# Kernel tuning notes

Measured on AMD Instinct MI355X. Metric: run time of the kernel, lower is better.

## Reference

```python
import jax, jax.numpy as jnp
import numpy as np

B, N, C, H = 4, 2048, 1024, 16
D = C // H  # head_dim = 64
SCALE = D ** -0.5


def setup_inputs() -> dict:
    key = jax.random.key(0)
    ks = jax.random.split(key, 7)
    # freqs_cis = exp(i*theta): unit-modulus rotations, as in standard RoPE
    theta = jax.random.uniform(ks[1], (B, N, D // 2), jnp.float32, 0.0, 2 * np.pi)
    return {
        "x": jax.random.normal(ks[0], (B, N, C), jnp.float32),
        "freqs_cos": jnp.cos(theta),
        "freqs_sin": jnp.sin(theta),
        "attn_mask": jax.random.normal(ks[2], (1, 1, N, N), jnp.float32) * 0.1,
        "Wqkv": jax.random.normal(ks[3], (3 * C, C), jnp.float32) * (C ** -0.5),
        "Wproj": jax.random.normal(ks[4], (C, C), jnp.float32) * (C ** -0.5),
        "bproj": jnp.zeros((C,), jnp.float32),
    }


def _rope(t, cos, sin):
    # t: [B,H,N,D]; cos/sin: [B,1,N,D/2]; complex multiply on interleaved pairs
    tr = t.reshape(*t.shape[:-1], D // 2, 2)
    t0, t1 = tr[..., 0], tr[..., 1]
    out = jnp.stack([t0 * cos - t1 * sin, t0 * sin + t1 * cos], axis=-1)
    return out.reshape(t.shape)


def reference(x, freqs_cos, freqs_sin, attn_mask, Wqkv, Wproj, bproj):
    qkv = x @ Wqkv.T  # [B,N,3C]
    qkv = qkv.reshape(B, N, 3, H, D).transpose(2, 0, 3, 1, 4)  # [3,B,H,N,D]
    q, k, v = qkv[0], qkv[1], qkv[2]
    cos = freqs_cos[:, None]  # [B,1,N,D/2]
    sin = freqs_sin[:, None]
    q = _rope(q, cos, sin)
    k = _rope(k, cos, sin)
    attn = jnp.einsum("bhnd,bhmd->bhnm", q * SCALE, k) + attn_mask
    attn = jax.nn.softmax(attn, axis=-1)
    out = jnp.einsum("bhnm,bhmd->bhnd", attn, v)  # [B,H,N,D]
    out = out.transpose(0, 2, 1, 3).reshape(B, N, C)
    return out @ Wproj.T + bproj
```

## Files before the change

### kernel.cpp

```cpp
#include <hip/hip_runtime.h>
#include <hip/hip_bf16.h>
#include <stdint.h>


typedef __bf16 bf16;
typedef __bf16 bf16x4 __attribute__((ext_vector_type(4)));
typedef __bf16 bf16x8 __attribute__((ext_vector_type(8)));
typedef float  f32x4  __attribute__((ext_vector_type(4)));
typedef float  f32x16 __attribute__((ext_vector_type(16)));
typedef int    int4v  __attribute__((ext_vector_type(4)));

#define MFMA16(a, b, c) __builtin_amdgcn_mfma_f32_16x16x32_bf16((a), (b), (c), 0, 0, 0)
#define MFMA32(a, b, c) __builtin_amdgcn_mfma_f32_32x32x16_bf16((a), (b), (c), 0, 0, 0)

__device__ __forceinline__ bf16x4 cvt4s(float a, float b, float c, float d) {
  bf16x4 r;
  r[0] = (bf16)a; r[1] = (bf16)b; r[2] = (bf16)c; r[3] = (bf16)d;
  return r;
}
__device__ __forceinline__ bf16x8 cvt8(f32x4 a, f32x4 b) {
  bf16x8 r;
  r[0] = (bf16)a[0]; r[1] = (bf16)a[1]; r[2] = (bf16)a[2]; r[3] = (bf16)a[3];
  r[4] = (bf16)b[0]; r[5] = (bf16)b[1]; r[6] = (bf16)b[2]; r[7] = (bf16)b[3];
  return r;
}
__device__ __forceinline__ void gload16(const void* g, void* l) {
  __builtin_amdgcn_global_load_lds((const __attribute__((address_space(1))) void*)g,
                                   (__attribute__((address_space(3))) void*)l, 16, 0, 0);
}

__global__ __launch_bounds__(256)
void cvt_all(const float* __restrict__ x,  bf16* __restrict__ xb,
             const float* __restrict__ wq, bf16* __restrict__ wqb,
             const float* __restrict__ wp, bf16* __restrict__ wpb,
             const float* __restrict__ mk, bf16* __restrict__ mkb)
{
  const int bi = blockIdx.x;
  const float* src; bf16* dst; float scale = 1.0f; size_t off;
  if (bi < 4096)      { src = x;  dst = xb;  off = (size_t)bi * 2048; }
  else if (bi < 5632) { src = wq; dst = wqb; off = (size_t)(bi - 4096) * 2048; }
  else if (bi < 6144) { src = wp; dst = wpb; off = (size_t)(bi - 5632) * 2048; }
  else { src = mk; dst = mkb; off = (size_t)(bi - 6144) * 2048;
         scale = 1.4426950408889634f; }
  const size_t i = off + (size_t)threadIdx.x * 8;
  f32x4 a = *(const f32x4*)(src + i) * scale;
  f32x4 b = *(const f32x4*)(src + i + 4) * scale;
  *(bf16x8*)(dst + i) = cvt8(a, b);
}

template<int MODE>
__global__ __launch_bounds__(256)
void gemm_bt(const bf16* __restrict__ A, const bf16* __restrict__ B,
             void* __restrict__ O0, bf16* __restrict__ O1, bf16* __restrict__ O2,
             const float* __restrict__ bias)
{
  constexpr int K = 1024;
  __shared__ __attribute__((aligned(16))) bf16 S[MODE == 0 ? 17408 : 16384];
  bf16* As = S;
  bf16* Bs = S + 128 * 64;
  const int tid = threadIdx.x, lane = tid & 63, wid = tid >> 6;
  const int m0 = blockIdx.x * 128, n0 = blockIdx.y * 128;
  const int wm = (wid >> 1) * 64, wn = (wid & 1) * 64;
  const int l15 = lane & 15, lg = lane >> 4;

  f32x4 acc[4][4] = {};

  for (int k0 = 0; k0 < K; k0 += 64) {
#pragma unroll
    for (int c = 0; c < 4; ++c) {
      const int seg = wid * 4 + c;
      const int o = seg * 1024 + lane * 16;
      const int row = o >> 7, colb = o & 127;
      gload16((const char*)B + (((size_t)(n0 + row) * K + k0) << 1) + colb,
              (char*)Bs + seg * 1024);
      gload16((const char*)A + (((size_t)(m0 + row) * K + k0) << 1) + colb,
              (char*)As + seg * 1024);
    }
    __syncthreads();

    bf16x8 af[4][2], bb[4][2];
#pragma unroll
    for (int i = 0; i < 4; ++i)
#pragma unroll
      for (int kk = 0; kk < 2; ++kk) {
        af[i][kk] = *(const bf16x8*)(As + (wm + i * 16 + l15) * 64 + kk * 32 + lg * 8);
        bb[i][kk] = *(const bf16x8*)(Bs + (wn + i * 16 + l15) * 64 + kk * 32 + lg * 8);
      }
#pragma unroll
    for (int mi = 0; mi < 4; ++mi)
#pragma unroll
      for (int ni = 0; ni < 4; ++ni)
#pragma unroll
        for (int kk = 0; kk < 2; ++kk)
          acc[mi][ni] = MFMA16(af[mi][kk], bb[ni][kk], acc[mi][ni]);
    __syncthreads();
  }

  if (MODE == 0) {
    bf16* T = S;
#pragma unroll
    for (int mi = 0; mi < 4; ++mi)
#pragma unroll
      for (int ni = 0; ni < 4; ++ni)
#pragma unroll
        for (int r = 0; r < 4; ++r)
          T[(wm + mi * 16 + lg * 4 + r) * 136 + wn + ni * 16 + l15] =
              (bf16)acc[mi][ni][r];
    __syncthreads();

    const int s = n0 >> 10;
    const int h0 = (n0 >> 6) & 15;
    if (s < 2) {
      bf16* dst = (s == 0) ? (bf16*)O0 : O1;
      const int nl = tid >> 1, ch = (tid & 1) * 64;
      const int row = m0 + nl, b = row >> 11, n = row & 2047;
#pragma unroll
      for (int j = 0; j < 8; ++j) {
        const int c = ch + j * 8;
        const int h = h0 + (c >> 6), d0 = c & 63;
        const int ds = (s == 1) ? (d0 ^ ((n & 7) << 3)) : d0;
        *(int4v*)(dst + (((size_t)(b * 16 + h) * 2048) + n) * 64 + ds) =
            *(const int4v*)(T + nl * 136 + c);
      }
    } else {
      const int c = tid >> 1, nh = (tid & 1) * 64;
      const int h = h0 + (c >> 6), d = c & 63;
      const int b = m0 >> 11, nb = m0 & 2047;
#pragma unroll
      for (int j = 0; j < 8; ++j) {
        const int n8 = nh + j * 8;
        __attribute__((aligned(16))) bf16 tmp[8];
#pragma unroll
        for (int i = 0; i < 8; ++i) tmp[i] = T[(n8 + i) * 136 + c];
        const int ng = nb + n8;
        const int nswz = (ng & ~63) | ((ng & 63) ^ ((d & 7) << 3));
        *(int4v*)(O2 + ((size_t)(b * 16 + h) * 64 + d) * 2048 + nswz) =
            *(const int4v*)tmp;
      }
    }
  } else {
#pragma unroll
    for (int mi = 0; mi < 4; ++mi)
#pragma unroll
      for (int ni = 0; ni < 4; ++ni)
#pragma unroll
        for (int r = 0; r < 4; ++r) {
          const int row = m0 + wm + mi * 16 + lg * 4 + r;
          const int col = n0 + wn + ni * 16 + l15;
          ((float*)O0)[(size_t)row * 1024 + col] = acc[mi][ni][r] + bias[col];
        }
  }
}

__global__ __launch_bounds__(256)
void rope_k(bf16* __restrict__ Q, bf16* __restrict__ K,
            const float* __restrict__ C, const float* __restrict__ S)
{
  constexpr float SL = 0.125f * 1.4426950408889634f;
  const int gid = blockIdx.x * 256 + threadIdx.x;
  const int part = gid & 3;
  const int rowid = gid >> 2;
  const int n = rowid & 2047;
  const int b = rowid >> 15;
  const size_t cb0 = ((size_t)(b * 2048 + n)) * 32;

  __attribute__((aligned(16))) bf16 buf[16];

  {
    float cf[8], sf[8];
    *(f32x4*)cf = *(const f32x4*)(C + cb0 + part * 8);
    *(f32x4*)(cf + 4) = *(const f32x4*)(C + cb0 + part * 8 + 4);
    *(f32x4*)sf = *(const f32x4*)(S + cb0 + part * 8);
    *(f32x4*)(sf + 4) = *(const f32x4*)(S + cb0 + part * 8 + 4);

    bf16* qp = Q + (size_t)rowid * 64 + part * 16;
    *(int4v*)buf = *(const int4v*)qp;
    *(int4v*)(buf + 8) = *(const int4v*)(qp + 8);
#pragma unroll
    for (int j = 0; j < 8; ++j) {
      const float t0 = (float)buf[2 * j], t1 = (float)buf[2 * j + 1];
      buf[2 * j]     = (bf16)((t0 * cf[j] - t1 * sf[j]) * SL);
      buf[2 * j + 1] = (bf16)((t0 * sf[j] + t1 * cf[j]) * SL);
    }
    *(int4v*)qp = *(int4v*)buf;
    *(int4v*)(qp + 8) = *(int4v*)(buf + 8);
  }

  {
    const int sg = n & 7;
    bf16* kp = K + (size_t)rowid * 64 + part * 16;
    *(int4v*)buf = *(const int4v*)kp;
    *(int4v*)(buf + 8) = *(const int4v*)(kp + 8);
#pragma unroll
    for (int gi = 0; gi < 2; ++gi) {
      const int lg = (2 * part + gi) ^ sg;
      const f32x4 c4 = *(const f32x4*)(C + cb0 + lg * 4);
      const f32x4 s4 = *(const f32x4*)(S + cb0 + lg * 4);
#pragma unroll
      for (int m = 0; m < 4; ++m) {
        const float t0 = (float)buf[gi * 8 + 2 * m];
        const float t1 = (float)buf[gi * 8 + 2 * m + 1];
        buf[gi * 8 + 2 * m]     = (bf16)(t0 * c4[m] - t1 * s4[m]);
        buf[gi * 8 + 2 * m + 1] = (bf16)(t0 * s4[m] + t1 * c4[m]);
      }
    }
    *(int4v*)kp = *(int4v*)buf;
    *(int4v*)(kp + 8) = *(int4v*)(buf + 8);
  }
}

template<int MM>
__global__ __launch_bounds__(512, 4)
void attn_k(const bf16* __restrict__ Q, const bf16* __restrict__ K,
            const bf16* __restrict__ VT, const void* __restrict__ Mv,
            bf16* __restrict__ O)
{
  constexpr float LOG2E = 1.4426950408889634f;
  constexpr int NT = 32;
  __shared__ __attribute__((aligned(16))) bf16 SH[18432];

  const int tid = threadIdx.x, lane = tid & 63, w = tid >> 6;
  const int bh = blockIdx.x;
  const int q0 = blockIdx.y * 256;
  const int b = bh >> 4, h = bh & 15;
  const int l31 = lane & 31, hi = lane >> 5;
  const int swz = (l31 & 7) << 3;

  const bf16* Qb = Q + (size_t)bh * 2048 * 64;
  const bf16* Kb = K + (size_t)bh * 2048 * 64;
  const bf16* Vb = VT + (size_t)bh * 64 * 2048;
  const float* Mqf = (const float*)Mv + (size_t)(q0 + w * 32 + l31) * 2048;
  const bf16*  Mqb = (const bf16*)Mv  + (size_t)(q0 + w * 32 + l31) * 2048;

  bf16x8 qf[4];
  {
    const bf16* qr = Qb + (size_t)(q0 + w * 32 + l31) * 64 + 8 * hi;
#pragma unroll
    for (int j = 0; j < 4; ++j) qf[j] = *(const bf16x8*)(qr + 16 * j);
  }

  f32x16 o[2] = {{0,0,0,0,0,0,0,0,0,0,0,0,0,0,0,0},
                 {0,0,0,0,0,0,0,0,0,0,0,0,0,0,0,0}};
  float li = 0.f;

#define STAGE_TILE(KVN, BUFSEL) do {                                          \
    bf16* Ktn = SH + (BUFSEL) * 8192;                                         \
    bf16* Vtn = Ktn + 4096;                                                   \
    gload16((const char*)Kb + (((size_t)(KVN) * 64 + tid * 8) << 1),          \
            (char*)Ktn + w * 1024);                                           \
    gload16((const char*)Vb +                                                 \
                (((size_t)(tid >> 3) * 2048 + (KVN) + (tid & 7) * 8) << 1),   \
            (char*)Vtn + w * 1024);                                           \
  } while (0)

  bf16x4 mkb_cur[2][4], mkb_nxt[2][4];

  STAGE_TILE(0, 0);
  if (MM == 1) {
#pragma unroll
    for (int sub = 0; sub < 2; ++sub)
#pragma unroll
      for (int rg = 0; rg < 4; ++rg)
        mkb_cur[sub][rg] = *(const bf16x4*)(Mqb + 32 * sub + 8 * rg + 4 * hi);
  }
  __syncthreads();

  for (int t = 0; t < NT; ++t) {
    bf16* Kt = SH + (t & 1) * 8192;
    bf16* Vt = Kt + 4096;

    if (t + 1 < NT) {
      const int kvn = (t + 1) * 64;
      STAGE_TILE(kvn, (t + 1) & 1);
      if (MM == 1) {
#pragma unroll
        for (int sub = 0; sub < 2; ++sub)
#pragma unroll
          for (int rg = 0; rg < 4; ++rg)
            mkb_nxt[sub][rg] = *(const bf16x4*)(Mqb + kvn + 32 * sub + 8 * rg + 4 * hi);
      }
    }
    f32x4 mkf[2][4];
    if (MM == 0) {
      const int kv0 = t * 64;
#pragma unroll
      for (int sub = 0; sub < 2; ++sub)
#pragma unroll
        for (int rg = 0; rg < 4; ++rg)
          mkf[sub][rg] = *(const f32x4*)(Mqf + kv0 + 32 * sub + 8 * rg + 4 * hi);
    }

#pragma unroll
    for (int sub = 0; sub < 2; ++sub) {
      f32x16 s;
#pragma unroll
      for (int rg = 0; rg < 4; ++rg)
#pragma unroll
        for (int i = 0; i < 4; ++i)
          s[4 * rg + i] = (MM == 0) ? mkf[sub][rg][i] * LOG2E
                                    : (float)mkb_cur[sub][rg][i];
      __builtin_amdgcn_s_setprio(1);
#pragma unroll
      for (int j = 0; j < 4; ++j) {
        const bf16x8 kf = *(const bf16x8*)(
            Kt + (sub * 32 + l31) * 64 + ((16 * j + 8 * hi) ^ swz));
        s = MFMA32(kf, qf[j], s);
      }
      __builtin_amdgcn_s_setprio(0);

      float rs = 0.f;
#pragma unroll
      for (int e = 0; e < 16; ++e) {
        const float p = __builtin_exp2f(s[e]);
        s[e] = p;
        rs += p;
      }
      rs += __shfl_xor(rs, 32);
      li += rs;

      uint32_t pk0, pk1, pk2, pk3, pk4, pk5, pk6, pk7;
      asm("v_cvt_pk_bf16_f32 %0, %1, %2" : "=v"(pk0) : "v"(s[0]),  "v"(s[1]));
      asm("v_cvt_pk_bf16_f32 %0, %1, %2" : "=v"(pk1) : "v"(s[2]),  "v"(s[3]));
      asm("v_cvt_pk_bf16_f32 %0, %1, %2" : "=v"(pk2) : "v"(s[4]),  "v"(s[5]));
      asm("v_cvt_pk_bf16_f32 %0, %1, %2" : "=v"(pk3) : "v"(s[6]),  "v"(s[7]));
      asm("v_cvt_pk_bf16_f32 %0, %1, %2" : "=v"(pk4) : "v"(s[8]),  "v"(s[9]));
      asm("v_cvt_pk_bf16_f32 %0, %1, %2" : "=v"(pk5) : "v"(s[10]), "v"(s[11]));
      asm("v_cvt_pk_bf16_f32 %0, %1, %2" : "=v"(pk6) : "v"(s[12]), "v"(s[13]));
      asm("v_cvt_pk_bf16_f32 %0, %1, %2" : "=v"(pk7) : "v"(s[14]), "v"(s[15]));
      asm("v_permlane32_swap_b32 %0, %1" : "+v"(pk0), "+v"(pk2));
      asm("v_permlane32_swap_b32 %0, %1" : "+v"(pk1), "+v"(pk3));
      asm("v_permlane32_swap_b32 %0, %1" : "+v"(pk4), "+v"(pk6));
      asm("v_permlane32_swap_b32 %0, %1" : "+v"(pk5), "+v"(pk7));
      uint32_t pau[2][4] = {{pk0, pk1, pk2, pk3}, {pk4, pk5, pk6, pk7}};
      bf16x8 pa[2];
      __builtin_memcpy(&pa[0], pau[0], 16);
      __builtin_memcpy(&pa[1], pau[1], 16);

      __builtin_amdgcn_s_setprio(1);
#pragma unroll
      for (int kh = 0; kh < 2; ++kh)
#pragma unroll
        for (int dblk = 0; dblk < 2; ++dblk) {
          const bf16x8 vf = *(const bf16x8*)(
              Vt + (dblk * 32 + l31) * 64 + ((sub * 32 + kh * 16 + 8 * hi) ^ swz));
          o[dblk] = MFMA32(vf, pa[kh], o[dblk]);
        }
      __builtin_amdgcn_s_setprio(0);
    }

    if (MM == 1 && t + 1 < NT) {
#pragma unroll
      for (int sub = 0; sub < 2; ++sub)
#pragma unroll
        for (int rg = 0; rg < 4; ++rg)
          mkb_cur[sub][rg] = mkb_nxt[sub][rg];
    }
    __syncthreads();
  }
#undef STAGE_TILE

  const float inv = 1.f / li;
  bf16* ow = SH + w * 2304;
#pragma unroll
  for (int dblk = 0; dblk < 2; ++dblk)
#pragma unroll
    for (int rg = 0; rg < 4; ++rg)
      *(bf16x4*)(ow + l31 * 72 + dblk * 32 + 8 * rg + 4 * hi) =
          cvt4s(o[dblk][4 * rg] * inv, o[dblk][4 * rg + 1] * inv,
                o[dblk][4 * rg + 2] * inv, o[dblk][4 * rg + 3] * inv);
  asm volatile("s_waitcnt lgkmcnt(0)" ::: "memory");
  __builtin_amdgcn_sched_barrier(0);
#pragma unroll
  for (int p = 0; p < 4; ++p) {
    const int row = p * 8 + (lane >> 3);
    const int n = q0 + w * 32 + row;
    const int4v v = *(const int4v*)(ow + row * 72 + (lane & 7) * 8);
    *(int4v*)(O + ((size_t)b * 2048 + n) * 1024 + h * 64 + (lane & 7) * 8) = v;
  }
}

extern "C" void kernel_launch(void* const* d_in, const int* in_sizes, int n_in,
                              void* d_out, int out_size, void* d_ws, size_t ws_size,
                              hipStream_t stream)
{
  (void)in_sizes; (void)n_in; (void)out_size;
  const float* x     = (const float*)d_in[0];
  const float* fcos  = (const float*)d_in[1];
  const float* fsin  = (const float*)d_in[2];
  const float* mask  = (const float*)d_in[3];
  const float* wqkv  = (const float*)d_in[4];
  const float* wproj = (const float*)d_in[5];
  const float* bproj = (const float*)d_in[6];
  float* out = (float*)d_out;

  const size_t SZ  = (size_t)64 * 2048 * 64 * 2;
  const size_t WQB = (size_t)3072 * 1024 * 2;
  const size_t WPB = (size_t)1024 * 1024 * 2;
  const size_t MKB = (size_t)2048 * 2048 * 2;
  const size_t BASE = 4 * SZ + WQB + WPB;
  if (ws_size < BASE) return;
  char* ws = (char*)d_ws;
  bf16* Qr  = (bf16*)(ws);
  bf16* Kr  = (bf16*)(ws + SZ);
  bf16* VT  = (bf16*)(ws + 2 * SZ);
  bf16* Ob  = (bf16*)(ws + 3 * SZ);
  bf16* Wqb = (bf16*)(ws + 4 * SZ);
  bf16* Wpb = (bf16*)(ws + 4 * SZ + WQB);
  bf16* Mb  = (bf16*)(ws + BASE);
  const bool useMb = (ws_size >= BASE + MKB);
  bf16* Xb = Ob;

  cvt_all<<<useMb ? 8192 : 6144, 256, 0, stream>>>(x, Xb, wqkv, Wqb,
                                                   wproj, Wpb, mask, Mb);
  gemm_bt<0><<<dim3(64, 24), 256, 0, stream>>>(Xb, Wqb, Qr, Kr, VT, nullptr);
  rope_k<<<2048, 256, 0, stream>>>(Qr, Kr, fcos, fsin);
  if (useMb)
    attn_k<1><<<dim3(64, 8), 512, 0, stream>>>(Qr, Kr, VT, Mb, Ob);
  else
    attn_k<0><<<dim3(64, 8), 512, 0, stream>>>(Qr, Kr, VT, mask, Ob);
  gemm_bt<1><<<dim3(64, 8), 256, 0, stream>>>(Ob, Wpb, out, nullptr, nullptr,
                                              bproj);
}
```

Before: 277.8 us.

## Remap GEMM blocks across XCDs and interleave both QK subtiles in attention

```diff
diff --git a/kernel.cpp b/kernel.cpp
--- a/kernel.cpp
+++ b/kernel.cpp
@@ -59,7 +59,9 @@
   bf16* As = S;
   bf16* Bs = S + 128 * 64;
   const int tid = threadIdx.x, lane = tid & 63, wid = tid >> 6;
-  const int m0 = blockIdx.x * 128, n0 = blockIdx.y * 128;
+  const int cpx = gridDim.x >> 3;
+  const int id  = ((int)blockIdx.x & 7) * cpx + ((int)blockIdx.x >> 3);
+  const int m0 = (id & 63) * 128, n0 = (id >> 6) * 128;
   const int wm = (wid >> 1) * 64, wn = (wid & 1) * 64;
   const int l15 = lane & 15, lg = lane >> 4;
 
@@ -253,6 +255,36 @@
             (char*)Vtn + w * 1024);                                           \
   } while (0)
 
+#define PV_BLOCK(SVEC, SUB) do {                                              \
+    uint32_t pk0, pk1, pk2, pk3, pk4, pk5, pk6, pk7;                          \
+    asm("v_cvt_pk_bf16_f32 %0, %1, %2" : "=v"(pk0) : "v"((SVEC)[0]),  "v"((SVEC)[1]));  \
+    asm("v_cvt_pk_bf16_f32 %0, %1, %2" : "=v"(pk1) : "v"((SVEC)[2]),  "v"((SVEC)[3]));  \
+    asm("v_cvt_pk_bf16_f32 %0, %1, %2" : "=v"(pk2) : "v"((SVEC)[4]),  "v"((SVEC)[5]));  \
+    asm("v_cvt_pk_bf16_f32 %0, %1, %2" : "=v"(pk3) : "v"((SVEC)[6]),  "v"((SVEC)[7]));  \
+    asm("v_cvt_pk_bf16_f32 %0, %1, %2" : "=v"(pk4) : "v"((SVEC)[8]),  "v"((SVEC)[9]));  \
+    asm("v_cvt_pk_bf16_f32 %0, %1, %2" : "=v"(pk5) : "v"((SVEC)[10]), "v"((SVEC)[11])); \
+    asm("v_cvt_pk_bf16_f32 %0, %1, %2" : "=v"(pk6) : "v"((SVEC)[12]), "v"((SVEC)[13])); \
+    asm("v_cvt_pk_bf16_f32 %0, %1, %2" : "=v"(pk7) : "v"((SVEC)[14]), "v"((SVEC)[15])); \
+    asm("v_permlane32_swap_b32 %0, %1" : "+v"(pk0), "+v"(pk2));               \
+    asm("v_permlane32_swap_b32 %0, %1" : "+v"(pk1), "+v"(pk3));               \
+    asm("v_permlane32_swap_b32 %0, %1" : "+v"(pk4), "+v"(pk6));               \
+    asm("v_permlane32_swap_b32 %0, %1" : "+v"(pk5), "+v"(pk7));               \
+    uint32_t pau[2][4] = {{pk0, pk1, pk2, pk3}, {pk4, pk5, pk6, pk7}};        \
+    bf16x8 pa[2];                                                             \
+    __builtin_memcpy(&pa[0], pau[0], 16);                                     \
+    __builtin_memcpy(&pa[1], pau[1], 16);                                     \
+    __builtin_amdgcn_s_setprio(1);                                            \
+    _Pragma("unroll")                                                         \
+    for (int kh = 0; kh < 2; ++kh)                                            \
+      _Pragma("unroll")                                                       \
+      for (int dblk = 0; dblk < 2; ++dblk) {                                  \
+        const bf16x8 vf = *(const bf16x8*)(                                   \
+            Vt + (dblk * 32 + l31) * 64 + (((SUB) * 32 + kh * 16 + 8 * hi) ^ swz)); \
+        o[dblk] = MFMA32(vf, pa[kh], o[dblk]);                                \
+      }                                                                       \
+    __builtin_amdgcn_s_setprio(0);                                            \
+  } while (0)
+
   bf16x4 mkb_cur[2][4], mkb_nxt[2][4];
 
   STAGE_TILE(0, 0);
@@ -290,63 +322,42 @@
           mkf[sub][rg] = *(const f32x4*)(Mqf + kv0 + 32 * sub + 8 * rg + 4 * hi);
     }
 
-#pragma unroll
-    for (int sub = 0; sub < 2; ++sub) {
-      f32x16 s;
-#pragma unroll
-      for (int rg = 0; rg < 4; ++rg)
-#pragma unroll
-        for (int i = 0; i < 4; ++i)
-          s[4 * rg + i] = (MM == 0) ? mkf[sub][rg][i] * LOG2E
-                                    : (float)mkb_cur[sub][rg][i];
-      __builtin_amdgcn_s_setprio(1);
-#pragma unroll
-      for (int j = 0; j < 4; ++j) {
-        const bf16x8 kf = *(const bf16x8*)(
-            Kt + (sub * 32 + l31) * 64 + ((16 * j + 8 * hi) ^ swz));
-        s = MFMA32(kf, qf[j], s);
-      }
-      __builtin_amdgcn_s_setprio(0);
-
-      float rs = 0.f;
-#pragma unroll
-      for (int e = 0; e < 16; ++e) {
-        const float p = __builtin_exp2f(s[e]);
-        s[e] = p;
-        rs += p;
-      }
-      rs += __shfl_xor(rs, 32);
-      li += rs;
-
-      uint32_t pk0, pk1, pk2, pk3, pk4, pk5, pk6, pk7;
-      asm("v_cvt_pk_bf16_f32 %0, %1, %2" : "=v"(pk0) : "v"(s[0]),  "v"(s[1]));
-      asm("v_cvt_pk_bf16_f32 %0, %1, %2" : "=v"(pk1) : "v"(s[2]),  "v"(s[3]));
-      asm("v_cvt_pk_bf16_f32 %0, %1, %2" : "=v"(pk2) : "v"(s[4]),  "v"(s[5]));
-      asm("v_cvt_pk_bf16_f32 %0, %1, %2" : "=v"(pk3) : "v"(s[6]),  "v"(s[7]));
-      asm("v_cvt_pk_bf16_f32 %0, %1, %2" : "=v"(pk4) : "v"(s[8]),  "v"(s[9]));
-      asm("v_cvt_pk_bf16_f32 %0, %1, %2" : "=v"(pk5) : "v"(s[10]), "v"(s[11]));
-      asm("v_cvt_pk_bf16_f32 %0, %1, %2" : "=v"(pk6) : "v"(s[12]), "v"(s[13]));
-      asm("v_cvt_pk_bf16_f32 %0, %1, %2" : "=v"(pk7) : "v"(s[14]), "v"(s[15]));
-      asm("v_permlane32_swap_b32 %0, %1" : "+v"(pk0), "+v"(pk2));
-      asm("v_permlane32_swap_b32 %0, %1" : "+v"(pk1), "+v"(pk3));
-      asm("v_permlane32_swap_b32 %0, %1" : "+v"(pk4), "+v"(pk6));
-      asm("v_permlane32_swap_b32 %0, %1" : "+v"(pk5), "+v"(pk7));
-      uint32_t pau[2][4] = {{pk0, pk1, pk2, pk3}, {pk4, pk5, pk6, pk7}};
-      bf16x8 pa[2];
-      __builtin_memcpy(&pa[0], pau[0], 16);
-      __builtin_memcpy(&pa[1], pau[1], 16);
-
-      __builtin_amdgcn_s_setprio(1);
-#pragma unroll
-      for (int kh = 0; kh < 2; ++kh)
-#pragma unroll
-        for (int dblk = 0; dblk < 2; ++dblk) {
-          const bf16x8 vf = *(const bf16x8*)(
-              Vt + (dblk * 32 + l31) * 64 + ((sub * 32 + kh * 16 + 8 * hi) ^ swz));
-          o[dblk] = MFMA32(vf, pa[kh], o[dblk]);
-        }
-      __builtin_amdgcn_s_setprio(0);
-    }
+    f32x16 s0, s1;
+#pragma unroll
+    for (int rg = 0; rg < 4; ++rg)
+#pragma unroll
+      for (int i = 0; i < 4; ++i) {
+        s0[4 * rg + i] = (MM == 0) ? mkf[0][rg][i] * LOG2E
+                                   : (float)mkb_cur[0][rg][i];
+        s1[4 * rg + i] = (MM == 0) ? mkf[1][rg][i] * LOG2E
+                                   : (float)mkb_cur[1][rg][i];
+      }
+    __builtin_amdgcn_s_setprio(1);
+#pragma unroll
+    for (int j = 0; j < 4; ++j) {
+      const int doff = (16 * j + 8 * hi) ^ swz;
+      const bf16x8 kf0 = *(const bf16x8*)(Kt + l31 * 64 + doff);
+      const bf16x8 kf1 = *(const bf16x8*)(Kt + (32 + l31) * 64 + doff);
+      s0 = MFMA32(kf0, qf[j], s0);
+      s1 = MFMA32(kf1, qf[j], s1);
+    }
+    __builtin_amdgcn_s_setprio(0);
+
+    float rs0 = 0.f, rs1 = 0.f;
+#pragma unroll
+    for (int e = 0; e < 16; ++e) {
+      const float p0 = __builtin_exp2f(s0[e]);
+      const float p1 = __builtin_exp2f(s1[e]);
+      s0[e] = p0; rs0 += p0;
+      s1[e] = p1; rs1 += p1;
+    }
+    rs0 += __shfl_xor(rs0, 32);
+    rs1 += __shfl_xor(rs1, 32);
+    li += rs0;
+    li += rs1;
+
+    PV_BLOCK(s0, 0);
+    PV_BLOCK(s1, 1);
 
     if (MM == 1 && t + 1 < NT) {
 #pragma unroll
@@ -358,6 +369,7 @@
     __syncthreads();
   }
 #undef STAGE_TILE
+#undef PV_BLOCK
 
   const float inv = 1.f / li;
   bf16* ow = SH + w * 2304;
@@ -412,12 +424,11 @@
 
   cvt_all<<<useMb ? 8192 : 6144, 256, 0, stream>>>(x, Xb, wqkv, Wqb,
                                                    wproj, Wpb, mask, Mb);
-  gemm_bt<0><<<dim3(64, 24), 256, 0, stream>>>(Xb, Wqb, Qr, Kr, VT, nullptr);
+  gemm_bt<0><<<1536, 256, 0, stream>>>(Xb, Wqb, Qr, Kr, VT, nullptr);
   rope_k<<<2048, 256, 0, stream>>>(Qr, Kr, fcos, fsin);
   if (useMb)
     attn_k<1><<<dim3(64, 8), 512, 0, stream>>>(Qr, Kr, VT, Mb, Ob);
   else
     attn_k<0><<<dim3(64, 8), 512, 0, stream>>>(Qr, Kr, VT, mask, Ob);
-  gemm_bt<1><<<dim3(64, 8), 256, 0, stream>>>(Ob, Wpb, out, nullptr, nullptr,
-                                              bproj);
-}
+  gemm_bt<1><<<512, 256, 0, stream>>>(Ob, Wpb, out, nullptr, nullptr, bproj);
+}
```

Measured after the change: 284.2 us. +2.3%, slower.
